# Optimization experiments

Hardware: AMD Instinct MI355X
Metric: run time of the kernel (lower is better)

Reference implementation:

```python
import jax, jax.numpy as jnp
import numpy as np

jax.config.update("jax_enable_x64", True)

VOCAB = 50257
GAMMA = 0.25
CW = 4              # context_width
HASH_KEY = 15485863
Z_CENTER = 2.0
TEMP = 2.0
P = 2147483647      # Mersenne prime 2**31 - 1 used as hash modulus
GREEN_SIZE = int(GAMMA * VOCAB)


def setup_inputs() -> dict:
    key = jax.random.key(0)
    k1, k2 = jax.random.split(key)
    B, S = 512, 8192
    token_ids = jax.random.randint(k1, (B, S), 0, VOCAB, dtype=jnp.int64)
    lengths = jax.random.randint(k2, (B,), 0, S, dtype=jnp.int64)
    dummy = jnp.zeros((1,), dtype=jnp.float32)  # mirrors non-trainable self._dummy
    return {"token_ids": token_ids, "lengths": lengths, "dummy": dummy}


def reference(token_ids, lengths, dummy):
    # KGW z-score detector, fully vectorized over (batch, seq).
    # Context hash: h_t = hash_key * prod_{i=1..CW} (tok_{t-i}+1)  (mod P)
    # Token t is "green" iff ((h_t * (tok_t+1)) mod P) mod VOCAB < gamma*VOCAB.
    tok = token_ids.astype(jnp.int64) + 1  # +1 avoids zero in the product
    B, S = tok.shape
    h = jnp.full((B, S), HASH_KEY % P, dtype=jnp.int64)
    for i in range(1, CW + 1):  # small fixed loop over context_width
        prev = jnp.pad(tok, ((0, 0), (i, 0)), constant_values=1)[:, :S]
        h = (h * prev) % P
    is_green = ((h * tok) % P) % VOCAB < GREEN_SIZE  # (B, S) bool

    pos = jnp.arange(S)
    valid = (pos[None, :] >= CW) & (pos[None, :] < lengths[:, None])
    count = jnp.sum(is_green & valid, axis=1).astype(jnp.float32)

    T = jnp.maximum(lengths - CW, 1).astype(jnp.float32)  # number of scored tokens
    z = (count - GAMMA * T) / jnp.sqrt(GAMMA * (1.0 - GAMMA) * T)
    reward = jax.nn.sigmoid((z - Z_CENTER) / TEMP)
    # sequences shorter than context_width+1 get reward 0
    reward = jnp.where(lengths >= CW + 1, reward, 0.0).astype(jnp.float32)
    return reward + 0.0 * jnp.sum(dummy)
```

## Files before the change

### kernel.cpp

```cpp
#include <hip/hip_runtime.h>


#define VOCAB 50257u
#define GREEN_SIZE 12564u
#define CW 4
#define HASH_KEY 15485863u
#define P31 2147483647u
#define SMAX 8192
#define BLK 1024

__device__ __forceinline__ unsigned int mulmodP_lazy(unsigned int a, unsigned int b) {
    unsigned long long x = (unsigned long long)a * (unsigned long long)b;
    unsigned int y = (unsigned int)(x & P31) + (unsigned int)(x >> 31);
    return (y & P31) + (y >> 31);
}

__global__ __launch_bounds__(BLK) void kgw_fused(
        const void* __restrict__ tokens, const void* __restrict__ lengths,
        float* __restrict__ out, int S) {
    __shared__ int s_tok[SMAX];
    __shared__ int s_red[BLK / 64];
    __shared__ int s_any;

    const int b   = blockIdx.x;
    const int tid = threadIdx.x;

    if (tid == 0) s_any = 0;
    __syncthreads();
    if (tid < 256 && ((const unsigned int*)tokens)[2 * tid + 1] != 0u)
        atomicOr(&s_any, 1);
    __syncthreads();
    const int is64 = (s_any == 0);

    const int Li = is64 ? (int)((const long long*)lengths)[b]
                        : ((const int*)lengths)[b];

    if (Li < CW + 1) {
        if (tid == 0) out[b] = 0.0f;
        return;
    }

    if (is64) {
        const longlong2* tp2 = (const longlong2*)((const long long*)tokens + (size_t)b * (size_t)S);
        const int npair = Li >> 1;
        for (int i = tid; i < npair; i += BLK) {
            longlong2 v = tp2[i];
            s_tok[2 * i]     = (int)v.x + 1;
            s_tok[2 * i + 1] = (int)v.y + 1;
        }
        if ((Li & 1) && tid == 0)
            s_tok[Li - 1] = (int)((const long long*)tokens)[(size_t)b * (size_t)S + Li - 1] + 1;
    } else {
        const int* tp = (const int*)tokens + (size_t)b * (size_t)S;
        const int4* tp4 = (const int4*)tp;
        const int nq = Li >> 2;
        for (int i = tid; i < nq; i += BLK) {
            int4 v = tp4[i];
            s_tok[4 * i]     = v.x + 1;
            s_tok[4 * i + 1] = v.y + 1;
            s_tok[4 * i + 2] = v.z + 1;
            s_tok[4 * i + 3] = v.w + 1;
        }
        for (int t = 4 * nq + tid; t < Li; t += BLK) s_tok[t] = tp[t] + 1;
    }
    __syncthreads();

    int cnt = 0;
    for (int t = CW + tid; t < Li; t += BLK) {
        unsigned int h = HASH_KEY;
        h = mulmodP_lazy(h, (unsigned int)s_tok[t - 1]);
        h = mulmodP_lazy(h, (unsigned int)s_tok[t - 2]);
        h = mulmodP_lazy(h, (unsigned int)s_tok[t - 3]);
        h = mulmodP_lazy(h, (unsigned int)s_tok[t - 4]);
        unsigned int g = mulmodP_lazy(h, (unsigned int)s_tok[t]);
        g = (g & P31) + (g >> 31);
        if (g >= P31) g -= P31;
        cnt += ((g % VOCAB) < GREEN_SIZE) ? 1 : 0;
    }

    for (int off = 32; off > 0; off >>= 1) cnt += __shfl_down(cnt, off, 64);
    if ((tid & 63) == 0) s_red[tid >> 6] = cnt;
    __syncthreads();

    if (tid == 0) {
        int c = 0;
        #pragma unroll
        for (int w = 0; w < BLK / 64; ++w) c += s_red[w];
        const float T = (float)(Li - CW);
        const float z = ((float)c - 0.25f * T) / sqrtf(0.1875f * T);
        out[b] = 1.0f / (1.0f + expf(-(z - 2.0f) * 0.5f));
    }
}

extern "C" void kernel_launch(void* const* d_in, const int* in_sizes, int n_in,
                              void* d_out, int out_size, void* d_ws, size_t ws_size,
                              hipStream_t stream) {
    const void* tokens  = d_in[0];
    const void* lengths = d_in[1];
    float* out = (float*)d_out;

    const int B = out_size;
    const int S = in_sizes[0] / B;

    kgw_fused<<<B, BLK, 0, stream>>>(tokens, lengths, out, S);
}
```

Before: 13.23 us.

## Load tokens directly into registers per thread, drop shared staging and barriers

Removes the 32KB shared-memory token buffer. Each thread now loads a contiguous window of 8+4 tokens straight from global memory into registers and computes 8 hashes, reusing the overlapping context within that window. The dtype probe becomes a per-wave ballot instead of a shared atomic guarded by two barriers. In exchange, neighbouring threads reload the 4-token overlap, and lower shared usage allows more resident blocks. The mul-mod order is reversed, which gives the same result because multiplication is commutative.

```diff
diff --git a/kernel.cpp b/kernel.cpp
--- a/kernel.cpp
+++ b/kernel.cpp
@@ -6,8 +6,8 @@
 #define CW 4
 #define HASH_KEY 15485863u
 #define P31 2147483647u
-#define SMAX 8192
 #define BLK 1024
+#define TPT 8
 
 __device__ __forceinline__ unsigned int mulmodP_lazy(unsigned int a, unsigned int b) {
     unsigned long long x = (unsigned long long)a * (unsigned long long)b;
@@ -18,19 +18,14 @@
 __global__ __launch_bounds__(BLK) void kgw_fused(
         const void* __restrict__ tokens, const void* __restrict__ lengths,
         float* __restrict__ out, int S) {
-    __shared__ int s_tok[SMAX];
     __shared__ int s_red[BLK / 64];
-    __shared__ int s_any;
 
-    const int b   = blockIdx.x;
-    const int tid = threadIdx.x;
+    const int b    = blockIdx.x;
+    const int tid  = threadIdx.x;
+    const int lane = tid & 63;
 
-    if (tid == 0) s_any = 0;
-    __syncthreads();
-    if (tid < 256 && ((const unsigned int*)tokens)[2 * tid + 1] != 0u)
-        atomicOr(&s_any, 1);
-    __syncthreads();
-    const int is64 = (s_any == 0);
+    const unsigned int probe = ((const unsigned int*)tokens)[2 * lane + 1];
+    const bool is64 = (__ballot(probe != 0u) == 0ull);
 
     const int Li = is64 ? (int)((const long long*)lengths)[b]
                         : ((const int*)lengths)[b];
@@ -40,46 +35,50 @@
         return;
     }
 
-    if (is64) {
-        const longlong2* tp2 = (const longlong2*)((const long long*)tokens + (size_t)b * (size_t)S);
-        const int npair = Li >> 1;
-        for (int i = tid; i < npair; i += BLK) {
-            longlong2 v = tp2[i];
-            s_tok[2 * i]     = (int)v.x + 1;
-            s_tok[2 * i + 1] = (int)v.y + 1;
+    const int t0 = CW + TPT * tid;
+    int cnt = 0;
+    if (t0 < Li) {
+        unsigned int tok[TPT + CW];
+        if (is64) {
+            const long long* row = (const long long*)tokens + (size_t)b * (size_t)S;
+            #pragma unroll
+            for (int k = 0; k < (TPT + CW) / 2; ++k) {
+                const int idx = TPT * tid + 2 * k;
+                const int vi  = min(idx, S - 2) >> 1;
+                const longlong2 v = ((const longlong2*)row)[vi];
+                tok[2 * k]     = (unsigned int)v.x + 1u;
+                tok[2 * k + 1] = (unsigned int)v.y + 1u;
+            }
+        } else {
+            const int* row = (const int*)tokens + (size_t)b * (size_t)S;
+            #pragma unroll
+            for (int k = 0; k < (TPT + CW) / 4; ++k) {
+                const int idx = TPT * tid + 4 * k;
+                const int vi  = min(idx, S - 4) >> 2;
+                const int4 v = ((const int4*)row)[vi];
+                tok[4 * k]     = (unsigned int)v.x + 1u;
+                tok[4 * k + 1] = (unsigned int)v.y + 1u;
+                tok[4 * k + 2] = (unsigned int)v.z + 1u;
+                tok[4 * k + 3] = (unsigned int)v.w + 1u;
+            }
         }
-        if ((Li & 1) && tid == 0)
-            s_tok[Li - 1] = (int)((const long long*)tokens)[(size_t)b * (size_t)S + Li - 1] + 1;
-    } else {
-        const int* tp = (const int*)tokens + (size_t)b * (size_t)S;
-        const int4* tp4 = (const int4*)tp;
-        const int nq = Li >> 2;
-        for (int i = tid; i < nq; i += BLK) {
-            int4 v = tp4[i];
-            s_tok[4 * i]     = v.x + 1;
-            s_tok[4 * i + 1] = v.y + 1;
-            s_tok[4 * i + 2] = v.z + 1;
-            s_tok[4 * i + 3] = v.w + 1;
+
+        #pragma unroll
+        for (int j = 0; j < TPT; ++j) {
+            unsigned int h = HASH_KEY;
+            h = mulmodP_lazy(h, tok[j]);
+            h = mulmodP_lazy(h, tok[j + 1]);
+            h = mulmodP_lazy(h, tok[j + 2]);
+            h = mulmodP_lazy(h, tok[j + 3]);
+            unsigned int g = mulmodP_lazy(h, tok[j + 4]);
+            g = (g & P31) + (g >> 31);
+            if (g >= P31) g -= P31;
+            cnt += ((t0 + j < Li) && ((g % VOCAB) < GREEN_SIZE)) ? 1 : 0;
         }
-        for (int t = 4 * nq + tid; t < Li; t += BLK) s_tok[t] = tp[t] + 1;
-    }
-    __syncthreads();
-
-    int cnt = 0;
-    for (int t = CW + tid; t < Li; t += BLK) {
-        unsigned int h = HASH_KEY;
-        h = mulmodP_lazy(h, (unsigned int)s_tok[t - 1]);
-        h = mulmodP_lazy(h, (unsigned int)s_tok[t - 2]);
-        h = mulmodP_lazy(h, (unsigned int)s_tok[t - 3]);
-        h = mulmodP_lazy(h, (unsigned int)s_tok[t - 4]);
-        unsigned int g = mulmodP_lazy(h, (unsigned int)s_tok[t]);
-        g = (g & P31) + (g >> 31);
-        if (g >= P31) g -= P31;
-        cnt += ((g % VOCAB) < GREEN_SIZE) ? 1 : 0;
     }
 
     for (int off = 32; off > 0; off >>= 1) cnt += __shfl_down(cnt, off, 64);
-    if ((tid & 63) == 0) s_red[tid >> 6] = cnt;
+    if (lane == 0) s_red[tid >> 6] = cnt;
     __syncthreads();
 
     if (tid == 0) {
```

New measurement: 12.44 us. 1.06x faster.
